# Kernel optimization log

Hardware: AMD Instinct MI355X
Metric: run time of the kernel (lower is better)

The kernel has to match this reference:

```python
import jax, jax.numpy as jnp
import numpy as np

N_HEADS = 16
D_EMBED = 1024
D_CROSS = 768
D_HEAD = D_EMBED // N_HEADS
B, S = 4, 2048


def setup_inputs() -> dict:
    key = jax.random.key(0)
    ks = jax.random.split(key, 10)
    sq = lambda k, shp, fan: jax.random.normal(k, shp, jnp.float32) / np.sqrt(fan)
    return {
        "x": jax.random.normal(ks[0], (B, S, D_EMBED), jnp.float32),
        "y": jax.random.normal(ks[1], (B, S, D_CROSS), jnp.float32),
        "Wq": sq(ks[2], (D_EMBED, D_EMBED), D_EMBED),
        "bq": jnp.zeros((D_EMBED,), jnp.float32),
        "Wk": sq(ks[3], (D_CROSS, D_EMBED), D_CROSS),
        "bk": jnp.zeros((D_EMBED,), jnp.float32),
        "Wv": sq(ks[4], (D_CROSS, D_EMBED), D_CROSS),
        "bv": jnp.zeros((D_EMBED,), jnp.float32),
        "Wo": sq(ks[5], (D_EMBED, D_EMBED), D_EMBED),
        "bo": jnp.zeros((D_EMBED,), jnp.float32),
    }


def reference(x, y, Wq, bq, Wk, bk, Wv, bv, Wo, bo):
    b, s, _ = y.shape
    q = x @ Wq + bq  # [b, s, d_embed]
    k = y @ Wk + bk
    v = y @ Wv + bv
    # [b, h, s, d_head]
    q = q.reshape(b, s, N_HEADS, D_HEAD).transpose(0, 2, 1, 3)
    k = k.reshape(b, s, N_HEADS, D_HEAD).transpose(0, 2, 1, 3)
    v = v.reshape(b, s, N_HEADS, D_HEAD).transpose(0, 2, 1, 3)
    scale = 1.0 / np.sqrt(D_HEAD).astype(np.float32)
    scores = jnp.einsum("bhqd,bhkd->bhqk", q, k) * scale
    weights = jax.nn.softmax(scores, axis=-1)
    out = jnp.einsum("bhqk,bhkd->bhqd", weights, v)
    out = out.transpose(0, 2, 1, 3).reshape(x.shape)
    return out @ Wo + bo
```

## Files before the change

kernel.cpp:

```cpp
#include <hip/hip_runtime.h>

#define NHEADS 16
#define DEMBED 1024
#define DCROSS 768
#define DHEAD  64
#define BATCH  4
#define SLEN   2048
#define MROWS  (BATCH * SLEN)

using bf16   = __bf16;
using bf16x8 = __attribute__((ext_vector_type(8))) __bf16;
using bf16x4 = __attribute__((ext_vector_type(4))) __bf16;
using f32x4  = __attribute__((ext_vector_type(4))) float;

__device__ __forceinline__ f32x4 mfma_bf16(bf16x8 a, bf16x8 b, f32x4 c) {
    return __builtin_amdgcn_mfma_f32_16x16x32_bf16(a, b, c, 0, 0, 0);
}

__device__ __forceinline__ void gl2lds16(const void* g, void* l) {
    __builtin_amdgcn_global_load_lds(
        (const __attribute__((address_space(1))) void*)g,
        (__attribute__((address_space(3))) void*)l, 16, 0, 0);
}

__global__ void cvt_xy(const float* __restrict__ x, const float* __restrict__ y,
                       bf16* __restrict__ xb, bf16* __restrict__ yb) {
    const int n4x = MROWS * DEMBED / 4;
    const int n4y = MROWS * DCROSS / 4;
    int i = blockIdx.x * blockDim.x + threadIdx.x;
    const float* src;
    bf16* dst;
    int j;
    if (i < n4x) { src = x; dst = xb; j = i; }
    else { j = i - n4x; if (j >= n4y) return; src = y; dst = yb; }
    float4 v = ((const float4*)src)[j];
    bf16x4 o = { (bf16)v.x, (bf16)v.y, (bf16)v.z, (bf16)v.w };
    ((bf16x4*)dst)[j] = o;
}

struct TrArgs { const float* src[4]; bf16* dst[4]; int K[4]; };
__global__ void transpose_all(TrArgs a) {
    __shared__ float tile[32][33];
    const int which = blockIdx.z;
    const int K = a.K[which];
    const int N = DEMBED;
    int n0 = blockIdx.x * 32, k0 = blockIdx.y * 32;
    if (k0 >= K) return;
    const float* W = a.src[which];
    bf16* Wt = a.dst[which];
    int tx = threadIdx.x, ty = threadIdx.y;
#pragma unroll
    for (int i = 0; i < 32; i += 8)
        tile[ty + i][tx] = W[(size_t)(k0 + ty + i) * N + n0 + tx];
    __syncthreads();
#pragma unroll
    for (int i = 0; i < 32; i += 8)
        Wt[(size_t)(n0 + ty + i) * K + k0 + tx] = (bf16)tile[tx][ty + i];
}

struct QkvArgs {
    const bf16 *xb, *yb, *Wqt, *Wkt, *Wvt;
    const float *bq, *bk, *bv;
    bf16 *Qb, *Kb, *Vt;
    float qscale;
};
__global__ __launch_bounds__(256, 3) void gemm_qkv(QkvArgs a) {
    __shared__ bf16 As[128 * 32];
    __shared__ bf16 Bs[128 * 32];
    const int id = blockIdx.x;
    const int cls = id >> 9;
    const bf16 *A, *Bt;
    const float* bias;
    int K, m0, n0;
    if (cls == 0) { int t = id;        m0 = (t >> 3) * 128; n0 = (t & 7) * 128;
                    A = a.xb;  Bt = a.Wqt; bias = a.bq; K = DEMBED; }
    else if (cls == 1) { int t = id - 512;  m0 = (t >> 3) * 128; n0 = (t & 7) * 128;
                    A = a.yb;  Bt = a.Wkt; bias = a.bk; K = DCROSS; }
    else { int t = id - 1024; m0 = (t >> 6) * 128; n0 = (t & 63) * 128;
                    A = a.Wvt; Bt = a.yb;  bias = a.bv; K = DCROSS; }

    const int tid  = threadIdx.x;
    const int wave = tid >> 6, lane = tid & 63;
    const int quad = lane >> 4, l15 = lane & 15;
    const int wr = wave >> 1, wc = wave & 1;

    const int trow = tid >> 2;
    const int tcol = ((tid & 3) ^ ((tid >> 3) & 3)) * 8;
    char* ldsA0 = (char*)As + wave * 1024;
    char* ldsB0 = (char*)Bs + wave * 1024;
    const bf16* gA0 = A + (size_t)(m0 + trow) * K + tcol;
    const bf16* gA1 = A + (size_t)(m0 + 64 + trow) * K + tcol;
    const bf16* gB0 = Bt + (size_t)(n0 + trow) * K + tcol;
    const bf16* gB1 = Bt + (size_t)(n0 + 64 + trow) * K + tcol;

    const int sw = (l15 >> 1) & 3;

    f32x4 acc[4][4] = {};

    for (int kt = 0; kt < K; kt += 32) {
        __syncthreads();
        gl2lds16(gA0 + kt, ldsA0);
        gl2lds16(gA1 + kt, ldsA0 + 4096);
        gl2lds16(gB0 + kt, ldsB0);
        gl2lds16(gB1 + kt, ldsB0 + 4096);
        __syncthreads();

        bf16x8 af[4], bfr[4];
#pragma unroll
        for (int i = 0; i < 4; i++)
            af[i] = *(const bf16x8*)((const char*)As +
                     (wr * 64 + i * 16 + l15) * 64 + ((quad ^ sw) * 16));
#pragma unroll
        for (int i = 0; i < 4; i++)
            bfr[i] = *(const bf16x8*)((const char*)Bs +
                     (wc * 64 + i * 16 + l15) * 64 + ((quad ^ sw) * 16));
#pragma unroll
        for (int fr = 0; fr < 4; fr++)
#pragma unroll
            for (int fc = 0; fc < 4; fc++)
                acc[fr][fc] = mfma_bf16(af[fr], bfr[fc], acc[fr][fc]);
    }

    if (cls < 2) {
        bf16* Cout = (cls == 0) ? a.Qb : a.Kb;
        const float alpha = (cls == 0) ? a.qscale : 1.0f;
#pragma unroll
        for (int fr = 0; fr < 4; fr++) {
            int row = m0 + wr * 64 + fr * 16 + quad * 4;
#pragma unroll
            for (int fc = 0; fc < 4; fc++) {
                int col = n0 + wc * 64 + fc * 16 + l15;
                float bv = bias[col];
#pragma unroll
                for (int r = 0; r < 4; r++)
                    Cout[(size_t)(row + r) * DEMBED + col] =
                        (bf16)((acc[fr][fc][r] + bv) * alpha);
            }
        }
    } else {
        const int b = n0 >> 11;
        const size_t bbase = (size_t)b * DEMBED * SLEN;
#pragma unroll
        for (int fr = 0; fr < 4; fr++) {
            int row = m0 + wr * 64 + fr * 16 + quad * 4;
#pragma unroll
            for (int fc = 0; fc < 4; fc++) {
                int col = n0 + wc * 64 + fc * 16 + l15;
                int s = col & (SLEN - 1);
#pragma unroll
                for (int r = 0; r < 4; r++)
                    a.Vt[bbase + (size_t)(row + r) * SLEN + s] =
                        (bf16)(acc[fr][fc][r] + bias[row + r]);
            }
        }
    }
}

__global__ __launch_bounds__(256, 4) void gemm_o(const bf16* __restrict__ A,
                                                 const bf16* __restrict__ Bt,
                                                 const float* __restrict__ bias,
                                                 float* __restrict__ Cout) {
    const int K = DEMBED, N = DEMBED;
    __shared__ bf16 As[128 * 32];
    __shared__ bf16 Bs[64 * 32];
    const int tid  = threadIdx.x;
    const int wave = tid >> 6, lane = tid & 63;
    const int quad = lane >> 4, l15 = lane & 15;
    const int m0 = blockIdx.x * 128, n0 = blockIdx.y * 64;

    const int trow = tid >> 2;
    const int tcol = ((tid & 3) ^ ((tid >> 3) & 3)) * 8;
    char* ldsA0 = (char*)As + wave * 1024;
    char* ldsB0 = (char*)Bs + wave * 1024;
    const bf16* gA0 = A + (size_t)(m0 + trow) * K + tcol;
    const bf16* gA1 = A + (size_t)(m0 + 64 + trow) * K + tcol;
    const bf16* gB0 = Bt + (size_t)(n0 + trow) * K + tcol;

    const int sw = (l15 >> 1) & 3;

    f32x4 acc[2][4] = {};

    for (int kt = 0; kt < K; kt += 32) {
        __syncthreads();
        gl2lds16(gA0 + kt, ldsA0);
        gl2lds16(gA1 + kt, ldsA0 + 4096);
        gl2lds16(gB0 + kt, ldsB0);
        __syncthreads();

        bf16x8 af[2], bfr[4];
#pragma unroll
        for (int i = 0; i < 2; i++)
            af[i] = *(const bf16x8*)((const char*)As +
                     (wave * 32 + i * 16 + l15) * 64 + ((quad ^ sw) * 16));
#pragma unroll
        for (int i = 0; i < 4; i++)
            bfr[i] = *(const bf16x8*)((const char*)Bs +
                     (i * 16 + l15) * 64 + ((quad ^ sw) * 16));
#pragma unroll
        for (int fr = 0; fr < 2; fr++)
#pragma unroll
            for (int fc = 0; fc < 4; fc++)
                acc[fr][fc] = mfma_bf16(af[fr], bfr[fc], acc[fr][fc]);
    }

#pragma unroll
    for (int fr = 0; fr < 2; fr++) {
        int row = m0 + wave * 32 + fr * 16 + quad * 4;
#pragma unroll
        for (int fc = 0; fc < 4; fc++) {
            int col = n0 + fc * 16 + l15;
            float bv = bias[col];
#pragma unroll
            for (int r = 0; r < 4; r++)
                Cout[(size_t)(row + r) * N + col] = acc[fr][fc][r] + bv;
        }
    }
}

__global__ __launch_bounds__(256, 4) void attn(const bf16* __restrict__ Q,
                                               const bf16* __restrict__ K,
                                               const bf16* __restrict__ Vt,
                                               bf16* __restrict__ O) {
    __shared__ bf16 KsA[64 * 64];
    __shared__ bf16 VsA[64 * 64];
    __shared__ bf16 PsA[4 * 32 * 72];

    const int tid  = threadIdx.x;
    const int wave = tid >> 6, lane = tid & 63;
    const int quad = lane >> 4, l15 = lane & 15;
    const int bh = blockIdx.y, b = bh >> 4, h = bh & 15;
    const size_t rowbase = (size_t)b * SLEN;
    const int qb = blockIdx.x * 128 + wave * 32;
    const int hc = h * DHEAD;

    bf16x8 qf[2][2];
#pragma unroll
    for (int rg = 0; rg < 2; rg++)
#pragma unroll
        for (int kg = 0; kg < 2; kg++)
            qf[rg][kg] = *(const bf16x8*)(Q + (rowbase + qb + rg * 16 + l15) * DEMBED
                                          + hc + kg * 32 + quad * 8);

    f32x4 o[2][4] = {};
    f32x4 lsv[2] = {};

    const bf16* Kbase = K + rowbase * DEMBED + hc;
    const bf16* Vbase = Vt + (size_t)bh * DHEAD * SLEN;

    const int xcol = (((tid & 7) ^ ((tid >> 3) & 7)) * 8);
    const bf16* gK = Kbase + (size_t)(tid >> 3) * DEMBED + xcol;
    const bf16* gV = Vbase + (size_t)(tid >> 3) * SLEN + xcol;
    char* ldsK = (char*)KsA + wave * 1024;
    char* ldsV = (char*)VsA + wave * 1024;
    bf16* Pw = PsA + wave * (32 * 72);

    for (int kb = 0; kb < SLEN; kb += 64) {
        __syncthreads();
        gl2lds16(gK + (size_t)kb * DEMBED, ldsK);
        gl2lds16(gK + (size_t)(kb + 32) * DEMBED, ldsK + 32 * 128);
        gl2lds16(gV + kb, ldsV);
        gl2lds16(gV + 32 * SLEN + kb, ldsV + 32 * 128);
        __syncthreads();

        f32x4 s[2][4] = {};
#pragma unroll
        for (int cg = 0; cg < 4; cg++)
#pragma unroll
            for (int kg = 0; kg < 2; kg++) {
                bf16x8 kf = *(const bf16x8*)((const char*)KsA +
                            (cg * 16 + l15) * 128 + (((kg * 4 + quad) ^ (l15 & 7)) * 16));
#pragma unroll
                for (int rg = 0; rg < 2; rg++)
                    s[rg][cg] = mfma_bf16(kf, qf[rg][kg], s[rg][cg]);
            }

#pragma unroll
        for (int rg = 0; rg < 2; rg++)
#pragma unroll
            for (int cg = 0; cg < 4; cg++) {
                f32x4 p;
                p[0] = __builtin_amdgcn_exp2f(s[rg][cg][0]);
                p[1] = __builtin_amdgcn_exp2f(s[rg][cg][1]);
                p[2] = __builtin_amdgcn_exp2f(s[rg][cg][2]);
                p[3] = __builtin_amdgcn_exp2f(s[rg][cg][3]);
                lsv[rg] += p;
                bf16x4 pb = { (bf16)p[0], (bf16)p[1], (bf16)p[2], (bf16)p[3] };
                *(bf16x4*)(Pw + (rg * 16 + l15) * 72 + cg * 16 + quad * 4) = pb;
            }

#pragma unroll
        for (int dg = 0; dg < 4; dg++)
#pragma unroll
            for (int kg = 0; kg < 2; kg++) {
                bf16x8 vf = *(const bf16x8*)((const char*)VsA +
                            (dg * 16 + l15) * 128 + (((kg * 4 + quad) ^ (l15 & 7)) * 16));
#pragma unroll
                for (int rg = 0; rg < 2; rg++)
                    o[rg][dg] = mfma_bf16(
                        *(const bf16x8*)(Pw + (rg * 16 + l15) * 72 + kg * 32 + quad * 8),
                        vf, o[rg][dg]);
            }
    }

    float inv[2];
#pragma unroll
    for (int rg = 0; rg < 2; rg++) {
        float rs = lsv[rg][0] + lsv[rg][1] + lsv[rg][2] + lsv[rg][3];
        rs += __shfl_xor(rs, 16);
        rs += __shfl_xor(rs, 32);
        inv[rg] = 1.0f / rs;
    }
#pragma unroll
    for (int rg = 0; rg < 2; rg++)
#pragma unroll
        for (int r = 0; r < 4; r++) {
            float iv = __shfl(inv[rg], quad * 4 + r);
#pragma unroll
            for (int dg = 0; dg < 4; dg++)
                O[(rowbase + qb + rg * 16 + quad * 4 + r) * DEMBED + hc + dg * 16 + l15] =
                    (bf16)(o[rg][dg][r] * iv);
        }
}

extern "C" void kernel_launch(void* const* d_in, const int* in_sizes, int n_in,
                              void* d_out, int out_size, void* d_ws, size_t ws_size,
                              hipStream_t stream) {
    const float* x  = (const float*)d_in[0];
    const float* y  = (const float*)d_in[1];
    const float* Wq = (const float*)d_in[2];
    const float* bq = (const float*)d_in[3];
    const float* Wk = (const float*)d_in[4];
    const float* bk = (const float*)d_in[5];
    const float* Wv = (const float*)d_in[6];
    const float* bv = (const float*)d_in[7];
    const float* Wo = (const float*)d_in[8];
    const float* bo = (const float*)d_in[9];
    float* out = (float*)d_out;

    char* ws = (char*)d_ws;
    size_t off = 0;
    auto alloc = [&](size_t bytes) {
        void* p = ws + off;
        off += (bytes + 255) & ~(size_t)255;
        return p;
    };
    bf16* xb  = (bf16*)alloc((size_t)MROWS * DEMBED * 2);
    bf16* yb  = (bf16*)alloc((size_t)MROWS * DCROSS * 2);
    bf16* Wqt = (bf16*)alloc((size_t)DEMBED * DEMBED * 2);
    bf16* Wkt = (bf16*)alloc((size_t)DEMBED * DCROSS * 2);
    bf16* Wvt = (bf16*)alloc((size_t)DEMBED * DCROSS * 2);
    bf16* Wot = (bf16*)alloc((size_t)DEMBED * DEMBED * 2);
    bf16* Qb  = (bf16*)alloc((size_t)MROWS * DEMBED * 2);
    bf16* Kb  = (bf16*)alloc((size_t)MROWS * DEMBED * 2);
    bf16* Vtb = (bf16*)alloc((size_t)MROWS * DEMBED * 2);
    bf16* Ab  = (bf16*)alloc((size_t)MROWS * DEMBED * 2);
    if (off > ws_size) return;

    {
        int n4 = MROWS * DEMBED / 4 + MROWS * DCROSS / 4;
        cvt_xy<<<(n4 + 255) / 256, 256, 0, stream>>>(x, y, xb, yb);
    }
    {
        TrArgs a;
        a.src[0] = Wq;  a.dst[0] = Wqt; a.K[0] = DEMBED;
        a.src[1] = Wk;  a.dst[1] = Wkt; a.K[1] = DCROSS;
        a.src[2] = Wv;  a.dst[2] = Wvt; a.K[2] = DCROSS;
        a.src[3] = Wo;  a.dst[3] = Wot; a.K[3] = DEMBED;
        transpose_all<<<dim3(32, 32, 4), dim3(32, 8), 0, stream>>>(a);
    }

    {
        QkvArgs a;
        a.xb = xb; a.yb = yb; a.Wqt = Wqt; a.Wkt = Wkt; a.Wvt = Wvt;
        a.bq = bq; a.bk = bk; a.bv = bv;
        a.Qb = Qb; a.Kb = Kb; a.Vt = Vtb;
        a.qscale = 0.125f * 1.4426950408889634f;
        gemm_qkv<<<1536, 256, 0, stream>>>(a);
    }

    attn<<<dim3(SLEN / 128, BATCH * NHEADS), 256, 0, stream>>>(Qb, Kb, Vtb, Ab);

    gemm_o<<<dim3(MROWS / 128, DEMBED / 64), 256, 0, stream>>>(Ab, Wot, bo, out);
}
```

Baseline: 303.2 us.

## Deepen GEMM K-tiles to 64, enlarge output GEMM tile, merge prep kernels, swap attention grid

The QKV and output GEMMs now load 64-wide K slices per barrier pair with an 8-way XOR swizzle, which halves the number of sync iterations. The output GEMM also moves from 128x64 to 128x128 tiles using a 2x2 wave layout and a lower occupancy bound. The weight transposes and x/y bf16 conversion are merged into a single launch, and the attention grid is reordered so blocks of the same query tile across heads are adjacent. The trade-offs are more LDS per block, lower occupancy in gemm_o, and fewer blocks in gemm_o.

```diff
diff --git a/kernel.cpp b/kernel.cpp
--- a/kernel.cpp
+++ b/kernel.cpp
@@ -23,39 +23,41 @@
         (__attribute__((address_space(3))) void*)l, 16, 0, 0);
 }
 
-__global__ void cvt_xy(const float* __restrict__ x, const float* __restrict__ y,
-                       bf16* __restrict__ xb, bf16* __restrict__ yb) {
-    const int n4x = MROWS * DEMBED / 4;
-    const int n4y = MROWS * DCROSS / 4;
-    int i = blockIdx.x * blockDim.x + threadIdx.x;
-    const float* src;
-    bf16* dst;
-    int j;
-    if (i < n4x) { src = x; dst = xb; j = i; }
-    else { j = i - n4x; if (j >= n4y) return; src = y; dst = yb; }
-    float4 v = ((const float4*)src)[j];
-    bf16x4 o = { (bf16)v.x, (bf16)v.y, (bf16)v.z, (bf16)v.w };
-    ((bf16x4*)dst)[j] = o;
-}
-
-struct TrArgs { const float* src[4]; bf16* dst[4]; int K[4]; };
-__global__ void transpose_all(TrArgs a) {
-    __shared__ float tile[32][33];
-    const int which = blockIdx.z;
-    const int K = a.K[which];
-    const int N = DEMBED;
-    int n0 = blockIdx.x * 32, k0 = blockIdx.y * 32;
-    if (k0 >= K) return;
-    const float* W = a.src[which];
-    bf16* Wt = a.dst[which];
-    int tx = threadIdx.x, ty = threadIdx.y;
-#pragma unroll
-    for (int i = 0; i < 32; i += 8)
-        tile[ty + i][tx] = W[(size_t)(k0 + ty + i) * N + n0 + tx];
-    __syncthreads();
-#pragma unroll
-    for (int i = 0; i < 32; i += 8)
-        Wt[(size_t)(n0 + ty + i) * K + k0 + tx] = (bf16)tile[tx][ty + i];
+struct PrepArgs {
+    const float* wsrc[4]; bf16* wdst[4]; int wK[4];
+    const float *x, *y; bf16 *xb, *yb;
+};
+#define NTRB 4096
+__global__ void prep_all(PrepArgs a) {
+    const int bid = blockIdx.x;
+    const int tid = threadIdx.x;
+    if (bid < NTRB) {
+        __shared__ float tile[32][33];
+        const int which = bid >> 10, rem = bid & 1023;
+        const int K = a.wK[which], N = DEMBED;
+        const int n0 = (rem & 31) * 32, k0 = (rem >> 5) * 32;
+        if (k0 >= K) return;
+        const float* W = a.wsrc[which];
+        bf16* Wt = a.wdst[which];
+        const int tx = tid & 31, ty = tid >> 5;
+#pragma unroll
+        for (int i = 0; i < 32; i += 8)
+            tile[ty + i][tx] = W[(size_t)(k0 + ty + i) * N + n0 + tx];
+        __syncthreads();
+#pragma unroll
+        for (int i = 0; i < 32; i += 8)
+            Wt[(size_t)(n0 + ty + i) * K + k0 + tx] = (bf16)tile[tx][ty + i];
+    } else {
+        const int n4x = MROWS * DEMBED / 4;
+        const int n4y = MROWS * DCROSS / 4;
+        int i = (bid - NTRB) * 256 + tid;
+        const float* src; bf16* dst; int j;
+        if (i < n4x) { src = a.x; dst = a.xb; j = i; }
+        else { j = i - n4x; if (j >= n4y) return; src = a.y; dst = a.yb; }
+        float4 v = ((const float4*)src)[j];
+        bf16x4 o = { (bf16)v.x, (bf16)v.y, (bf16)v.z, (bf16)v.w };
+        ((bf16x4*)dst)[j] = o;
+    }
 }
 
 struct QkvArgs {
@@ -65,8 +67,8 @@
     float qscale;
 };
 __global__ __launch_bounds__(256, 3) void gemm_qkv(QkvArgs a) {
-    __shared__ bf16 As[128 * 32];
-    __shared__ bf16 Bs[128 * 32];
+    __shared__ bf16 As[128 * 64];
+    __shared__ bf16 Bs[128 * 64];
     const int id = blockIdx.x;
     const int cls = id >> 9;
     const bf16 *A, *Bt;
@@ -84,41 +86,44 @@
     const int quad = lane >> 4, l15 = lane & 15;
     const int wr = wave >> 1, wc = wave & 1;
 
-    const int trow = tid >> 2;
-    const int tcol = ((tid & 3) ^ ((tid >> 3) & 3)) * 8;
+    const int srow = wave * 8 + (lane >> 3);
+    const int scol = ((lane & 7) ^ (lane >> 3)) * 8;
     char* ldsA0 = (char*)As + wave * 1024;
     char* ldsB0 = (char*)Bs + wave * 1024;
-    const bf16* gA0 = A + (size_t)(m0 + trow) * K + tcol;
-    const bf16* gA1 = A + (size_t)(m0 + 64 + trow) * K + tcol;
-    const bf16* gB0 = Bt + (size_t)(n0 + trow) * K + tcol;
-    const bf16* gB1 = Bt + (size_t)(n0 + 64 + trow) * K + tcol;
-
-    const int sw = (l15 >> 1) & 3;
+    const bf16* gA0 = A + (size_t)(m0 + srow) * K + scol;
+    const bf16* gB0 = Bt + (size_t)(n0 + srow) * K + scol;
+
+    const int sw = l15 & 7;
 
     f32x4 acc[4][4] = {};
 
-    for (int kt = 0; kt < K; kt += 32) {
-        __syncthreads();
-        gl2lds16(gA0 + kt, ldsA0);
-        gl2lds16(gA1 + kt, ldsA0 + 4096);
-        gl2lds16(gB0 + kt, ldsB0);
-        gl2lds16(gB1 + kt, ldsB0 + 4096);
-        __syncthreads();
-
-        bf16x8 af[4], bfr[4];
-#pragma unroll
-        for (int i = 0; i < 4; i++)
-            af[i] = *(const bf16x8*)((const char*)As +
-                     (wr * 64 + i * 16 + l15) * 64 + ((quad ^ sw) * 16));
-#pragma unroll
-        for (int i = 0; i < 4; i++)
-            bfr[i] = *(const bf16x8*)((const char*)Bs +
-                     (wc * 64 + i * 16 + l15) * 64 + ((quad ^ sw) * 16));
-#pragma unroll
-        for (int fr = 0; fr < 4; fr++)
-#pragma unroll
-            for (int fc = 0; fc < 4; fc++)
-                acc[fr][fc] = mfma_bf16(af[fr], bfr[fc], acc[fr][fc]);
+    for (int kt = 0; kt < K; kt += 64) {
+        __syncthreads();
+#pragma unroll
+        for (int c = 0; c < 4; c++)
+            gl2lds16(gA0 + (size_t)c * 32 * K + kt, ldsA0 + c * 4096);
+#pragma unroll
+        for (int c = 0; c < 4; c++)
+            gl2lds16(gB0 + (size_t)c * 32 * K + kt, ldsB0 + c * 4096);
+        __syncthreads();
+
+#pragma unroll
+        for (int kg = 0; kg < 2; kg++) {
+            bf16x8 af[4], bfr[4];
+#pragma unroll
+            for (int i = 0; i < 4; i++)
+                af[i] = *(const bf16x8*)((const char*)As +
+                         (wr * 64 + i * 16 + l15) * 128 + (((kg * 4 + quad) ^ sw) * 16));
+#pragma unroll
+            for (int i = 0; i < 4; i++)
+                bfr[i] = *(const bf16x8*)((const char*)Bs +
+                         (wc * 64 + i * 16 + l15) * 128 + (((kg * 4 + quad) ^ sw) * 16));
+#pragma unroll
+            for (int fr = 0; fr < 4; fr++)
+#pragma unroll
+                for (int fc = 0; fc < 4; fc++)
+                    acc[fr][fc] = mfma_bf16(af[fr], bfr[fc], acc[fr][fc]);
+        }
     }
 
     if (cls < 2) {
@@ -156,59 +161,65 @@
     }
 }
 
-__global__ __launch_bounds__(256, 4) void gemm_o(const bf16* __restrict__ A,
+__global__ __launch_bounds__(256, 3) void gemm_o(const bf16* __restrict__ A,
                                                  const bf16* __restrict__ Bt,
                                                  const float* __restrict__ bias,
                                                  float* __restrict__ Cout) {
     const int K = DEMBED, N = DEMBED;
-    __shared__ bf16 As[128 * 32];
-    __shared__ bf16 Bs[64 * 32];
+    __shared__ bf16 As[128 * 64];
+    __shared__ bf16 Bs[128 * 64];
     const int tid  = threadIdx.x;
     const int wave = tid >> 6, lane = tid & 63;
     const int quad = lane >> 4, l15 = lane & 15;
-    const int m0 = blockIdx.x * 128, n0 = blockIdx.y * 64;
-
-    const int trow = tid >> 2;
-    const int tcol = ((tid & 3) ^ ((tid >> 3) & 3)) * 8;
+    const int m0 = blockIdx.x * 128, n0 = blockIdx.y * 128;
+    const int wr = wave >> 1, wc = wave & 1;
+
+    const int srow = wave * 8 + (lane >> 3);
+    const int scol = ((lane & 7) ^ (lane >> 3)) * 8;
     char* ldsA0 = (char*)As + wave * 1024;
     char* ldsB0 = (char*)Bs + wave * 1024;
-    const bf16* gA0 = A + (size_t)(m0 + trow) * K + tcol;
-    const bf16* gA1 = A + (size_t)(m0 + 64 + trow) * K + tcol;
-    const bf16* gB0 = Bt + (size_t)(n0 + trow) * K + tcol;
-
-    const int sw = (l15 >> 1) & 3;
-
-    f32x4 acc[2][4] = {};
-
-    for (int kt = 0; kt < K; kt += 32) {
-        __syncthreads();
-        gl2lds16(gA0 + kt, ldsA0);
-        gl2lds16(gA1 + kt, ldsA0 + 4096);
-        gl2lds16(gB0 + kt, ldsB0);
-        __syncthreads();
-
-        bf16x8 af[2], bfr[4];
-#pragma unroll
-        for (int i = 0; i < 2; i++)
-            af[i] = *(const bf16x8*)((const char*)As +
-                     (wave * 32 + i * 16 + l15) * 64 + ((quad ^ sw) * 16));
-#pragma unroll
-        for (int i = 0; i < 4; i++)
-            bfr[i] = *(const bf16x8*)((const char*)Bs +
-                     (i * 16 + l15) * 64 + ((quad ^ sw) * 16));
-#pragma unroll
-        for (int fr = 0; fr < 2; fr++)
-#pragma unroll
-            for (int fc = 0; fc < 4; fc++)
-                acc[fr][fc] = mfma_bf16(af[fr], bfr[fc], acc[fr][fc]);
-    }
-
-#pragma unroll
-    for (int fr = 0; fr < 2; fr++) {
-        int row = m0 + wave * 32 + fr * 16 + quad * 4;
+    const bf16* gA0 = A + (size_t)(m0 + srow) * K + scol;
+    const bf16* gB0 = Bt + (size_t)(n0 + srow) * K + scol;
+
+    const int sw = l15 & 7;
+
+    f32x4 acc[4][4] = {};
+
+    for (int kt = 0; kt < K; kt += 64) {
+        __syncthreads();
+#pragma unroll
+        for (int c = 0; c < 4; c++)
+            gl2lds16(gA0 + (size_t)c * 32 * K + kt, ldsA0 + c * 4096);
+#pragma unroll
+        for (int c = 0; c < 4; c++)
+            gl2lds16(gB0 + (size_t)c * 32 * K + kt, ldsB0 + c * 4096);
+        __syncthreads();
+
+#pragma unroll
+        for (int kg = 0; kg < 2; kg++) {
+            bf16x8 af[4], bfr[4];
+#pragma unroll
+            for (int i = 0; i < 4; i++)
+                af[i] = *(const bf16x8*)((const char*)As +
+                         (wr * 64 + i * 16 + l15) * 128 + (((kg * 4 + quad) ^ sw) * 16));
+#pragma unroll
+            for (int i = 0; i < 4; i++)
+                bfr[i] = *(const bf16x8*)((const char*)Bs +
+                         (wc * 64 + i * 16 + l15) * 128 + (((kg * 4 + quad) ^ sw) * 16));
+#pragma unroll
+            for (int fr = 0; fr < 4; fr++)
+#pragma unroll
+                for (int fc = 0; fc < 4; fc++)
+                    acc[fr][fc] = mfma_bf16(af[fr], bfr[fc], acc[fr][fc]);
+        }
+    }
+
+#pragma unroll
+    for (int fr = 0; fr < 4; fr++) {
+        int row = m0 + wr * 64 + fr * 16 + quad * 4;
 #pragma unroll
         for (int fc = 0; fc < 4; fc++) {
-            int col = n0 + fc * 16 + l15;
+            int col = n0 + wc * 64 + fc * 16 + l15;
             float bv = bias[col];
 #pragma unroll
             for (int r = 0; r < 4; r++)
@@ -228,9 +239,9 @@
     const int tid  = threadIdx.x;
     const int wave = tid >> 6, lane = tid & 63;
     const int quad = lane >> 4, l15 = lane & 15;
-    const int bh = blockIdx.y, b = bh >> 4, h = bh & 15;
+    const int bh = blockIdx.x, b = bh >> 4, h = bh & 15;
     const size_t rowbase = (size_t)b * SLEN;
-    const int qb = blockIdx.x * 128 + wave * 32;
+    const int qb = blockIdx.y * 128 + wave * 32;
     const int hc = h * DHEAD;
 
     bf16x8 qf[2][2];
@@ -357,16 +368,14 @@
     if (off > ws_size) return;
 
     {
-        int n4 = MROWS * DEMBED / 4 + MROWS * DCROSS / 4;
-        cvt_xy<<<(n4 + 255) / 256, 256, 0, stream>>>(x, y, xb, yb);
-    }
-    {
-        TrArgs a;
-        a.src[0] = Wq;  a.dst[0] = Wqt; a.K[0] = DEMBED;
-        a.src[1] = Wk;  a.dst[1] = Wkt; a.K[1] = DCROSS;
-        a.src[2] = Wv;  a.dst[2] = Wvt; a.K[2] = DCROSS;
-        a.src[3] = Wo;  a.dst[3] = Wot; a.K[3] = DEMBED;
-        transpose_all<<<dim3(32, 32, 4), dim3(32, 8), 0, stream>>>(a);
+        PrepArgs a;
+        a.wsrc[0] = Wq; a.wdst[0] = Wqt; a.wK[0] = DEMBED;
+        a.wsrc[1] = Wk; a.wdst[1] = Wkt; a.wK[1] = DCROSS;
+        a.wsrc[2] = Wv; a.wdst[2] = Wvt; a.wK[2] = DCROSS;
+        a.wsrc[3] = Wo; a.wdst[3] = Wot; a.wK[3] = DEMBED;
+        a.x = x; a.y = y; a.xb = xb; a.yb = yb;
+        int ncvt = (MROWS * DEMBED / 4 + MROWS * DCROSS / 4 + 255) / 256;
+        prep_all<<<NTRB + ncvt, 256, 0, stream>>>(a);
     }
 
     {
@@ -378,7 +387,7 @@
         gemm_qkv<<<1536, 256, 0, stream>>>(a);
     }
 
-    attn<<<dim3(SLEN / 128, BATCH * NHEADS), 256, 0, stream>>>(Qb, Kb, Vtb, Ab);
-
-    gemm_o<<<dim3(MROWS / 128, DEMBED / 64), 256, 0, stream>>>(Ab, Wot, bo, out);
-}
+    attn<<<dim3(BATCH * NHEADS, SLEN / 128), 256, 0, stream>>>(Qb, Kb, Vtb, Ab);
+
+    gemm_o<<<dim3(MROWS / 128, DEMBED / 128), 256, 0, stream>>>(Ab, Wot, bo, out);
+}
```

Measured after the change: 286.4 us. 5.5% less time.
